# Kernel optimization log

Measured on AMD Instinct MI355X. Metric: run time of the kernel, lower is better.

The kernel has to match this reference:

```python
import jax, jax.numpy as jnp
import numpy as np

EM_DIM = 64
GROUP = 16
DIM_IN = 1024


def _position_embedding(boxes, part_boxes):
    # boxes: [N,4], part_boxes: [P,4] -> [N,P,EM_DIM]
    xmin, ymin, xmax, ymax = [boxes[:, i:i + 1] for i in range(4)]            # [N,1]
    pxmin, pymin, pxmax, pymax = [part_boxes[:, i:i + 1].T for i in range(4)]  # [1,P]
    bw = xmax - xmin + 1.0
    bh = ymax - ymin + 1.0
    pw = pxmax - pxmin + 1.0
    ph = pymax - pymin + 1.0
    cx = 0.5 * (xmin + xmax)
    cy = 0.5 * (ymin + ymax)
    pcx = 0.5 * (pxmin + pxmax)
    pcy = 0.5 * (pymin + pymax)
    dx = jnp.abs((cx - pcx) / bw)
    dy = jnp.abs((cy - pcy) / bh)
    dx = jnp.log(jnp.where(dx < 1e-3, 1e-3, dx))
    dy = jnp.log(jnp.where(dy < 1e-3, 1e-3, dy))
    dw = jnp.log(pw / bw)
    dh = jnp.log(ph / bh)
    pos = jnp.stack([dx, dy, dw, dh], axis=2)                                  # [N,P,4]
    em_range = jnp.arange(EM_DIM // 8, dtype=pos.dtype) / (EM_DIM // 8)        # [8]
    em_mat = jnp.power(jnp.asarray(1000.0, pos.dtype), em_range)               # [8]
    div = (100.0 * pos)[..., None] / em_mat                                    # [N,P,4,8]
    emb = jnp.concatenate([jnp.sin(div), jnp.cos(div)], axis=3)                # [N,P,4,16]
    return emb.reshape(pos.shape[0], pos.shape[1], EM_DIM)


def _single_relation(boxes, part_boxes, bf, pf, Wg_w, Wg_b, Wq_w, Wq_b, Wk_w, Wk_b, conv_w, conv_b):
    N = bf.shape[0]
    P = pf.shape[0]
    emb = _position_embedding(boxes, part_boxes)                               # [N,P,64]
    pos_feat = jax.nn.relu(emb @ Wg_w.T + Wg_b)                                # [N,P,G]
    att_weight = jnp.transpose(pos_feat, (0, 2, 1))                            # [N,G,P]
    q = (bf @ Wq_w.T + Wq_b).reshape(N, GROUP, EM_DIM)                         # [N,G,64]
    k = (pf @ Wk_w.T + Wk_b).reshape(P, GROUP, EM_DIM)                         # [P,G,64]
    att = jnp.einsum('ngd,pgd->ngp', q, k) * (1.0 / GROUP)                     # [N,G,P]
    att_weight = jnp.where(att_weight < 1e-6, 1e-6, att_weight)
    sm = jax.nn.softmax(jnp.log(att_weight) + att, axis=2)                     # [N,G,P]
    out = jnp.einsum('ngp,pc->ngc', sm, pf)                                    # [N,G,dim_in]
    # grouped 1x1 conv: group g maps dim_in channels -> EM_DIM channels
    w3 = conv_w.reshape(GROUP, EM_DIM, DIM_IN)
    rel = jnp.einsum('ngc,goc->ngo', out, w3).reshape(N, GROUP * EM_DIM) + conv_b
    return rel                                                                  # [N, G*EM_DIM]


def setup_inputs() -> dict:
    key = jax.random.key(0)
    ks = jax.random.split(key, 12)
    N_TOT, P_TOT = 2048, 2048

    def make_rois(k1, k2, n, n1):
        xy = jax.random.uniform(k1, (n, 2), jnp.float32) * 800.0
        wh = jax.random.uniform(k2, (n, 2), jnp.float32) * 200.0 + 16.0
        boxes = jnp.concatenate([xy, xy + wh], axis=1)
        idx = jnp.concatenate([jnp.zeros((n1, 1)), jnp.ones((n - n1, 1))], axis=0).astype(jnp.float32)
        return jnp.concatenate([idx, boxes], axis=1)

    rois = make_rois(ks[0], ks[1], N_TOT, 1024)
    part_rois = make_rois(ks[2], ks[3], P_TOT, 1024)
    box_feats = jax.random.normal(ks[4], (N_TOT, DIM_IN), jnp.float32)
    part_feats = jax.random.normal(ks[5], (P_TOT, DIM_IN), jnp.float32)
    xav_g = float(np.sqrt(6.0 / (EM_DIM + GROUP)))
    xav_qk = float(np.sqrt(6.0 / (DIM_IN + GROUP * EM_DIM)))
    Wg_w = jax.random.uniform(ks[6], (GROUP, EM_DIM), jnp.float32, -xav_g, xav_g)
    Wg_b = jnp.zeros((GROUP,), jnp.float32)
    Wq_w = jax.random.uniform(ks[7], (GROUP * EM_DIM, DIM_IN), jnp.float32, -xav_qk, xav_qk)
    Wq_b = jnp.zeros((GROUP * EM_DIM,), jnp.float32)
    Wk_w = jax.random.uniform(ks[8], (GROUP * EM_DIM, DIM_IN), jnp.float32, -xav_qk, xav_qk)
    Wk_b = jnp.zeros((GROUP * EM_DIM,), jnp.float32)
    conv_w = jax.random.normal(ks[9], (GROUP * EM_DIM, DIM_IN), jnp.float32) * 0.02
    conv_b = jnp.zeros((GROUP * EM_DIM,), jnp.float32)
    return {"rois": rois, "part_rois": part_rois, "box_feats": box_feats,
            "part_feats": part_feats, "Wg_w": Wg_w, "Wg_b": Wg_b,
            "Wq_w": Wq_w, "Wq_b": Wq_b, "Wk_w": Wk_w, "Wk_b": Wk_b,
            "conv_w": conv_w, "conv_b": conv_b, "n1_boxes": 1024, "n1_parts": 1024}


def reference(rois, part_rois, box_feats, part_feats, Wg_w, Wg_b, Wq_w, Wq_b,
              Wk_w, Wk_b, conv_w, conv_b, n1_boxes, n1_parts):
    boxes = rois[:, 1:5]
    part_boxes = part_rois[:, 1:5]
    params = (Wg_w, Wg_b, Wq_w, Wq_b, Wk_w, Wk_b, conv_w, conv_b)
    rel1 = _single_relation(boxes[:n1_boxes], part_boxes[:n1_parts],
                            box_feats[:n1_boxes], part_feats[:n1_parts], *params)
    rel2 = _single_relation(boxes[n1_boxes:], part_boxes[n1_parts:],
                            box_feats[n1_boxes:], part_feats[n1_parts:], *params)
    return jnp.concatenate([rel1, rel2], axis=0)  # [N_total, GROUP*EM_DIM]
```

## Files before the change

### kernel.cpp

```cpp
#include <hip/hip_runtime.h>

typedef unsigned short u16;
using short8  = __attribute__((ext_vector_type(8))) short;
using float4v = __attribute__((ext_vector_type(4))) float;

__device__ __forceinline__ u16 f2bf(float f) {
    union { float f; unsigned u; } v; v.f = f;
    unsigned r = (v.u + 0x7fff + ((v.u >> 16) & 1)) >> 16;
    return (u16)r;
}
__device__ __forceinline__ float bf2f(u16 h) {
    union { unsigned u; float f; } v; v.u = ((unsigned)h) << 16; return v.f;
}
__device__ __forceinline__ unsigned pkbf(float lo, float hi) {
    unsigned d;
    asm("v_cvt_pk_bf16_f32 %0, %1, %2" : "=v"(d) : "v"(lo), "v"(hi));
    return d;
}
__device__ __forceinline__ float sin_rev(float r) {
    float f, s;
    asm("v_fract_f32 %0, %1" : "=v"(f) : "v"(r));
    asm("v_sin_f32 %0, %1" : "=v"(s) : "v"(f));
    return s;
}
__device__ __forceinline__ void dma16(const void* g, void* l) {
    __builtin_amdgcn_global_load_lds((const __attribute__((address_space(1))) void*)g,
                                     (__attribute__((address_space(3))) void*)l, 16, 0, 0);
}

__device__ __forceinline__ void cvt4(const float* __restrict__ s, u16* __restrict__ o, int i) {
    float4 v = ((const float4*)s)[i];
    uint2 r; r.x = pkbf(v.x, v.y); r.y = pkbf(v.z, v.w);
    ((uint2*)o)[i] = r;
}

__global__ __launch_bounds__(256)
void cvt_all(const float* __restrict__ s0, const float* __restrict__ s1,
             const float* __restrict__ s2, const float* __restrict__ s3,
             const float* __restrict__ s4, const float* __restrict__ prois,
             u16* __restrict__ o0, u16* __restrict__ o1, u16* __restrict__ o2,
             u16* __restrict__ o3, u16* __restrict__ o4, float4* __restrict__ PD,
             int na4, int nb4, int nw4, int PT) {
    int i = blockIdx.x * 256 + threadIdx.x;
    if (i < na4) { cvt4(s0, o0, i); return; }
    i -= na4;
    if (i < nb4) { cvt4(s1, o1, i); return; }
    i -= nb4;
    if (i < nw4) { cvt4(s2, o2, i); return; }
    i -= nw4;
    if (i < nw4) { cvt4(s3, o3, i); return; }
    i -= nw4;
    if (i < nw4) { cvt4(s4, o4, i); return; }
    i -= nw4;
    if (i < PT) {
        const float* pr = prois + (size_t)i * 5;
        float pxmin = pr[1], pymin = pr[2], pxmax = pr[3], pymax = pr[4];
        PD[i] = make_float4(0.5f * (pxmin + pxmax), 0.5f * (pymin + pymax),
                            __logf(pxmax - pxmin + 1.0f), __logf(pymax - pymin + 1.0f));
    }
}

__global__ __launch_bounds__(256)
void proj_mfma(const u16* __restrict__ Ab, const u16* __restrict__ Pb,
               const u16* __restrict__ Wqb, const u16* __restrict__ Wkb,
               const u16* __restrict__ Cwb, const float* __restrict__ bq,
               const float* __restrict__ bk, u16* __restrict__ Qb,
               u16* __restrict__ Kb, u16* __restrict__ PVt, int PT) {
    __shared__ __align__(16) u16 As[128 * 64];
    __shared__ __align__(16) u16 Ws[64 * 64];
    __shared__ __align__(16) u16 Tr[128 * 68];

    const int z = blockIdx.z;
    const int m0 = blockIdx.y * 128, j0 = blockIdx.x * 64;
    const u16* A = (z == 0) ? Ab : Pb;
    const u16* W = (z == 0) ? Wqb : (z == 1 ? Wkb : Cwb);
    const int t = threadIdx.x;
    const int w = t >> 6, lane = t & 63;
    const int wm = w >> 1, wn = w & 1;
    const int lr = lane >> 3, lc = lane & 7, gch = lc ^ lr;
    const int fm = lane & 15, quad = lane >> 4;

    float4v zero4 = {0.f, 0.f, 0.f, 0.f};
    float4v acc[4][2];
#pragma unroll
    for (int i = 0; i < 4; ++i) { acc[i][0] = zero4; acc[i][1] = zero4; }

    for (int k0 = 0; k0 < 1024; k0 += 64) {
#pragma unroll
        for (int i = 0; i < 4; ++i) {
            int row = w * 32 + i * 8 + lr;
            dma16(A + (size_t)(m0 + row) * 1024 + k0 + gch * 8,
                  As + (w * 32 + i * 8) * 64 + lane * 8);
        }
#pragma unroll
        for (int i = 0; i < 2; ++i) {
            int row = w * 16 + i * 8 + lr;
            dma16(W + (size_t)(j0 + row) * 1024 + k0 + gch * 8,
                  Ws + (w * 16 + i * 8) * 64 + lane * 8);
        }
        __syncthreads();
#pragma unroll
        for (int ks = 0; ks < 2; ++ks) {
            int c = ks * 4 + quad;
            short8 af[4], bf[2];
#pragma unroll
            for (int i = 0; i < 4; ++i) {
                int ra = wm * 64 + i * 16 + fm;
                af[i] = *(const short8*)(As + ra * 64 + ((c ^ (ra & 7)) * 8));
            }
#pragma unroll
            for (int j = 0; j < 2; ++j) {
                int rb = wn * 32 + j * 16 + fm;
                bf[j] = *(const short8*)(Ws + rb * 64 + ((c ^ (rb & 7)) * 8));
            }
#pragma unroll
            for (int i = 0; i < 4; ++i)
#pragma unroll
                for (int j = 0; j < 2; ++j)
                    acc[i][j] = __builtin_amdgcn_mfma_f32_16x16x32_bf16(af[i], bf[j], acc[i][j], 0, 0, 0);
        }
        __syncthreads();
    }

    if (z < 2) {
        u16* O = z ? Kb : Qb;
        const float* bias = z ? bk : bq;
#pragma unroll
        for (int j = 0; j < 2; ++j) {
            int jl = wn * 32 + j * 16 + fm;
            float bb = bias[j0 + jl];
#pragma unroll
            for (int i = 0; i < 4; ++i) {
                int mlb = wm * 64 + i * 16 + quad * 4;
#pragma unroll
                for (int r = 0; r < 4; ++r)
                    Tr[(mlb + r) * 68 + jl] = f2bf(acc[i][j][r] + bb);
            }
        }
        __syncthreads();
#pragma unroll
        for (int i2 = 0; i2 < 4; ++i2) {
            int f = i2 * 2048 + t * 8;
            int ml = f >> 6, jl = f & 63;
            union { uint2 u2[2]; short8 s8; } uu;
            uu.u2[0] = *(const uint2*)(Tr + ml * 68 + jl);
            uu.u2[1] = *(const uint2*)(Tr + ml * 68 + jl + 4);
            *(short8*)(O + (size_t)(m0 + ml) * 1024 + j0 + jl) = uu.s8;
        }
    } else {
#pragma unroll
        for (int j = 0; j < 2; ++j) {
            int jl = wn * 32 + j * 16 + fm;
#pragma unroll
            for (int i = 0; i < 4; ++i) {
                int mlb = wm * 64 + i * 16 + quad * 4;
                uint2 pk;
                pk.x = pkbf(acc[i][j][0], acc[i][j][1]);
                pk.y = pkbf(acc[i][j][2], acc[i][j][3]);
                *(uint2*)(Tr + jl * 136 + mlb) = pk;
            }
        }
        __syncthreads();
#pragma unroll
        for (int i2 = 0; i2 < 4; ++i2) {
            int f = i2 * 2048 + t * 8;
            int jl = f >> 7, ml = f & 127;
            union { uint2 u2[2]; short8 s8; } uu;
            uu.u2[0] = *(const uint2*)(Tr + jl * 136 + ml);
            uu.u2[1] = *(const uint2*)(Tr + jl * 136 + ml + 4);
            *(short8*)(PVt + (size_t)(j0 + jl) * PT + m0 + ml) = uu.s8;
        }
    }
}

__global__ __launch_bounds__(256)
void att_mfma(const u16* __restrict__ Qb, const u16* __restrict__ Kb,
              u16* __restrict__ ATT, const int* __restrict__ n1b_p,
              const int* __restrict__ n1p_p, int PT) {
    __shared__ __align__(16) u16 Qs[128 * 64];
    __shared__ __align__(16) u16 Ks[128 * 64];
    __shared__ __align__(16) u16 Tr[128 * 130];

    const int g = blockIdx.z;
    const int n0 = blockIdx.y * 128, pl0 = blockIdx.x * 128;
    const int n1b = *n1b_p, n1p = *n1p_p;
    const int hh = (n0 >= n1b) ? 1 : 0;
    const int p0 = hh ? n1p : 0;
    const int Ph = hh ? (PT - n1p) : n1p;
    if (pl0 >= Ph) return;
    const int t = threadIdx.x;
    const int w = t >> 6, lane = t & 63;
    const int wm = w >> 1, wn = w & 1;
    const int lr = lane >> 3, lc = lane & 7, gch = lc ^ lr;
    const int fm = lane & 15, quad = lane >> 4;

    float4v zero4 = {0.f, 0.f, 0.f, 0.f};
    float4v acc[4][4];
#pragma unroll
    for (int i = 0; i < 4; ++i)
#pragma unroll
        for (int j = 0; j < 4; ++j) acc[i][j] = zero4;

#pragma unroll
    for (int i = 0; i < 4; ++i) {
        int row = w * 32 + i * 8 + lr;
        dma16(Qb + (size_t)(n0 + row) * 1024 + g * 64 + gch * 8,
              Qs + (w * 32 + i * 8) * 64 + lane * 8);
        dma16(Kb + (size_t)(p0 + pl0 + row) * 1024 + g * 64 + gch * 8,
              Ks + (w * 32 + i * 8) * 64 + lane * 8);
    }
    __syncthreads();
#pragma unroll
    for (int ks = 0; ks < 2; ++ks) {
        int c = ks * 4 + quad;
        short8 af[4], bf[4];
#pragma unroll
        for (int i = 0; i < 4; ++i) {
            int ra = wm * 64 + i * 16 + fm;
            af[i] = *(const short8*)(Qs + ra * 64 + ((c ^ (ra & 7)) * 8));
            int rb = wn * 64 + i * 16 + fm;
            bf[i] = *(const short8*)(Ks + rb * 64 + ((c ^ (rb & 7)) * 8));
        }
#pragma unroll
        for (int i = 0; i < 4; ++i)
#pragma unroll
            for (int j = 0; j < 4; ++j)
                acc[i][j] = __builtin_amdgcn_mfma_f32_16x16x32_bf16(af[i], bf[j], acc[i][j], 0, 0, 0);
    }
#pragma unroll
    for (int j = 0; j < 4; ++j) {
        int pl = wn * 64 + j * 16 + fm;
#pragma unroll
        for (int i = 0; i < 4; ++i)
#pragma unroll
            for (int r = 0; r < 4; ++r) {
                int nl = wm * 64 + i * 16 + quad * 4 + r;
                Tr[nl * 130 + pl] = f2bf(__expf(acc[i][j][r] * 0.0625f));
            }
    }
    __syncthreads();
#pragma unroll
    for (int i = 0; i < 8; ++i) {
        int f = i * 2048 + t * 8;
        int nl = f >> 7, pl = f & 127;
        short8 v = *(const short8*)(Tr + nl * 130 + pl);
        *(short8*)(ATT + ((size_t)(n0 + nl) * 16 + g) * 1024 + pl0 + pl) = v;
    }
}

__global__ __launch_bounds__(256)
void softmax_fused(const float* __restrict__ rois, const float4* __restrict__ PD,
                   const float* __restrict__ Wg_w, const float* __restrict__ Wg_b,
                   u16* __restrict__ ATT, float* __restrict__ INV,
                   const int* __restrict__ n1b_p, const int* __restrict__ n1p_p, int PT) {
    __shared__ float redl[4][16];

    const int n = blockIdx.x, t = threadIdx.x;
    const int w = t >> 6, lane = t & 63;
    const int fm = lane & 15, quad = lane >> 4;
    const int n1b = *n1b_p, n1p = *n1p_p;
    const int hh = (n >= n1b) ? 1 : 0;
    const int p0 = hh ? n1p : 0;
    const int Ph = hh ? (PT - n1p) : n1p;

    float xmin = rois[n * 5 + 1], ymin = rois[n * 5 + 2];
    float xmax = rois[n * 5 + 3], ymax = rois[n * 5 + 4];
    float bw = xmax - xmin + 1.0f, bh = ymax - ymin + 1.0f;
    float cx = 0.5f * (xmin + xmax), cy = 0.5f * (ymin + ymax);

    const int jA = quad >> 1, trig = quad & 1;
    float cA   = (jA == 0) ? cx : cy;
    float invA = (jA == 0) ? (1.0f / bw) : (1.0f / bh);
    float lB   = (jA == 0) ? __logf(bw) : __logf(bh);
    float toff = trig ? 0.25f : 0.0f;

    const int g_ = fm;
    short8 b1, b2;
    {
        const float* w1 = Wg_w + g_ * 64 + quad * 8;
        const float* w2 = Wg_w + g_ * 64 + 32 + quad * 8;
        unsigned* p1 = (unsigned*)&b1;
        unsigned* p2 = (unsigned*)&b2;
#pragma unroll
        for (int kk = 0; kk < 4; ++kk) {
            p1[kk] = pkbf(w1[2 * kk], w1[2 * kk + 1]);
            p2[kk] = pkbf(w2[2 * kk], w2[2 * kk + 1]);
        }
    }
    float wgb = Wg_b[g_];

    const float inv_em[8] = {1.0f, 0.4216965034f, 0.1778279410f, 0.0749894209f,
                             0.0316227766f, 0.0133352143f, 0.0056234133f, 0.0023713737f};
    const float REV = 15.91549431f;
    const int prange = Ph >> 2;
    const int pb0 = w * prange;
    float ssum = 0.0f;
    u16* rowp = ATT + ((size_t)n * 16 + g_) * 1024;

    float4 pd_c = PD[p0 + pb0 + fm];
    ushort4 ea_c = *(const ushort4*)(rowp + pb0 + quad * 4);

#pragma unroll 2
    for (int pt = 0; pt < 16; ++pt) {
        int pbase = pb0 + pt * 16;
        float4 pd_n;
        ushort4 ea_n;
        if (pt < 15) {
            pd_n = PD[p0 + pbase + 16 + fm];
            ea_n = *(const ushort4*)(rowp + pbase + 16 + quad * 4);
        }
        float pc = (jA == 0) ? pd_c.x : pd_c.y;
        float lp = (jA == 0) ? pd_c.z : pd_c.w;
        float posA = __logf(fmaxf(fabsf(cA - pc) * invA, 0.001f));
        float posB = lp - lB;
        float br1 = posA * REV, br2 = posB * REV;
        float e1[8], e2[8];
#pragma unroll
        for (int k = 0; k < 8; ++k) {
            e1[k] = sin_rev(fmaf(br1, inv_em[k], toff));
            e2[k] = sin_rev(fmaf(br2, inv_em[k], toff));
        }
        short8 a1, a2;
        unsigned* pa1 = (unsigned*)&a1;
        unsigned* pa2 = (unsigned*)&a2;
#pragma unroll
        for (int kk = 0; kk < 4; ++kk) {
            pa1[kk] = pkbf(e1[2 * kk], e1[2 * kk + 1]);
            pa2[kk] = pkbf(e2[2 * kk], e2[2 * kk + 1]);
        }
        float4v acc = {wgb, wgb, wgb, wgb};
        acc = __builtin_amdgcn_mfma_f32_16x16x32_bf16(a1, b1, acc, 0, 0, 0);
        acc = __builtin_amdgcn_mfma_f32_16x16x32_bf16(a2, b2, acc, 0, 0, 0);

        float w0  = fmaxf(acc[0], 1e-6f) * bf2f(ea_c.x);
        float w1v = fmaxf(acc[1], 1e-6f) * bf2f(ea_c.y);
        float w2v = fmaxf(acc[2], 1e-6f) * bf2f(ea_c.z);
        float w3v = fmaxf(acc[3], 1e-6f) * bf2f(ea_c.w);
        ssum += (w0 + w1v) + (w2v + w3v);
        uint2 wp; wp.x = pkbf(w0, w1v); wp.y = pkbf(w2v, w3v);
        *(uint2*)(rowp + pbase + quad * 4) = wp;

        pd_c = pd_n;
        ea_c = ea_n;
    }

    ssum += __shfl_xor(ssum, 16, 64);
    ssum += __shfl_xor(ssum, 32, 64);
    if (lane < 16) redl[w][lane] = ssum;
    __syncthreads();
    if (t < 16)
        INV[(size_t)n * 16 + t] = 1.0f / (redl[0][t] + redl[1][t] + redl[2][t] + redl[3][t]);
}

__global__ __launch_bounds__(256)
void rel_mfma(const u16* __restrict__ SM, const u16* __restrict__ PVt,
              const float* __restrict__ conv_b, const float* __restrict__ INV,
              float* __restrict__ OUT, const int* __restrict__ n1b_p,
              const int* __restrict__ n1p_p, int PT) {
    __shared__ __align__(16) u16 As[64 * 64];
    __shared__ __align__(16) u16 Bs[64 * 64];

    const int n0 = blockIdx.x * 64, g = blockIdx.y;
    const int n1b = *n1b_p, n1p = *n1p_p;
    const int hh = (n0 >= n1b) ? 1 : 0;
    const int p0 = hh ? n1p : 0;
    const int Ph = hh ? (PT - n1p) : n1p;
    const int t = threadIdx.x;
    const int w = t >> 6, lane = t & 63;
    const int wm = w >> 1, wn = w & 1;
    const int lr = lane >> 3, lc = lane & 7, gch = lc ^ lr;
    const int fm = lane & 15, quad = lane >> 4;

    float4v zero4 = {0.f, 0.f, 0.f, 0.f};
    float4v acc[2][2];
#pragma unroll
    for (int i = 0; i < 2; ++i) { acc[i][0] = zero4; acc[i][1] = zero4; }

    for (int k0 = 0; k0 < Ph; k0 += 64) {
#pragma unroll
        for (int i = 0; i < 2; ++i) {
            int row = w * 16 + i * 8 + lr;
            dma16(SM + ((size_t)(n0 + row) * 16 + g) * 1024 + k0 + gch * 8,
                  As + (w * 16 + i * 8) * 64 + lane * 8);
            dma16(PVt + (size_t)(g * 64 + row) * PT + p0 + k0 + gch * 8,
                  Bs + (w * 16 + i * 8) * 64 + lane * 8);
        }
        __syncthreads();
#pragma unroll
        for (int ks = 0; ks < 2; ++ks) {
            int c = ks * 4 + quad;
            short8 af[2], bf[2];
#pragma unroll
            for (int i = 0; i < 2; ++i) {
                int ra = wm * 32 + i * 16 + fm;
                af[i] = *(const short8*)(As + ra * 64 + ((c ^ (ra & 7)) * 8));
                int rb = wn * 32 + i * 16 + fm;
                bf[i] = *(const short8*)(Bs + rb * 64 + ((c ^ (rb & 7)) * 8));
            }
#pragma unroll
            for (int i = 0; i < 2; ++i)
#pragma unroll
                for (int j = 0; j < 2; ++j)
                    acc[i][j] = __builtin_amdgcn_mfma_f32_16x16x32_bf16(af[i], bf[j], acc[i][j], 0, 0, 0);
        }
        __syncthreads();
    }
    float bb[2];
    bb[0] = conv_b[g * 64 + wn * 32 + fm];
    bb[1] = conv_b[g * 64 + wn * 32 + 16 + fm];
#pragma unroll
    for (int i = 0; i < 2; ++i)
#pragma unroll
        for (int r = 0; r < 4; ++r) {
            int nn = n0 + wm * 32 + i * 16 + quad * 4 + r;
            float iv = INV[(size_t)nn * 16 + g];
#pragma unroll
            for (int j = 0; j < 2; ++j) {
                int o = wn * 32 + j * 16 + fm;
                OUT[(size_t)nn * 1024 + g * 64 + o] = acc[i][j][r] * iv + bb[j];
            }
        }
}

extern "C" void kernel_launch(void* const* d_in, const int* in_sizes, int n_in,
                              void* d_out, int out_size, void* d_ws, size_t ws_size,
                              hipStream_t stream) {
    const float* rois   = (const float*)d_in[0];
    const float* prois  = (const float*)d_in[1];
    const float* bfeat  = (const float*)d_in[2];
    const float* pfeat  = (const float*)d_in[3];
    const float* Wg_w   = (const float*)d_in[4];
    const float* Wg_b   = (const float*)d_in[5];
    const float* Wq_w   = (const float*)d_in[6];
    const float* Wq_b   = (const float*)d_in[7];
    const float* Wk_w   = (const float*)d_in[8];
    const float* Wk_b   = (const float*)d_in[9];
    const float* conv_w = (const float*)d_in[10];
    const float* conv_b = (const float*)d_in[11];
    const int*   n1b    = (const int*)d_in[12];
    const int*   n1p    = (const int*)d_in[13];

    const int NT = in_sizes[2] / 1024;
    const int PT = in_sizes[3] / 1024;

    u16* ATT = (u16*)d_ws;
    u16* Qb  = ATT + (size_t)NT * 16 * 1024;
    u16* Kb  = Qb + (size_t)NT * 1024;
    u16* PVt = Kb + (size_t)PT * 1024;
    float* INVp = (float*)(PVt + (size_t)1024 * PT);
    float4* PD  = (float4*)(INVp + (size_t)NT * 16);
    u16* Ab  = ATT;
    u16* Pb  = Ab + (size_t)NT * 1024;
    u16* Wqb = Pb + (size_t)PT * 1024;
    u16* Wkb = Wqb + 1024 * 1024;
    u16* Cwb = Wkb + 1024 * 1024;

    dim3 blk(256);
    int nf4 = NT * 1024 / 4, pf4 = PT * 1024 / 4, wf4 = 1024 * 1024 / 4;
    int tot = nf4 + pf4 + 3 * wf4 + PT;
    cvt_all<<<dim3((tot + 255) / 256), blk, 0, stream>>>(
        bfeat, pfeat, Wq_w, Wk_w, conv_w, prois, Ab, Pb, Wqb, Wkb, Cwb, PD,
        nf4, pf4, wf4, PT);

    proj_mfma<<<dim3(16, NT / 128, 3), blk, 0, stream>>>(Ab, Pb, Wqb, Wkb, Cwb,
                                                         Wq_b, Wk_b, Qb, Kb, PVt, PT);
    att_mfma<<<dim3(PT / 128, NT / 128, 16), blk, 0, stream>>>(Qb, Kb, ATT, n1b, n1p, PT);
    softmax_fused<<<dim3(NT), blk, 0, stream>>>(rois, PD, Wg_w, Wg_b, ATT, INVp, n1b, n1p, PT);
    rel_mfma<<<dim3(NT / 64, 16), blk, 0, stream>>>(ATT, PVt, conv_b, INVp,
                                                    (float*)d_out, n1b, n1p, PT);
}
```

Measured before the change: 202.8 us.

## Stage softmax attention row in LDS via async DMA and double block size

The softmax_fused kernel now copies each box's full 16x1024 bf16 attention block into shared memory with dma16 async copies at kernel start. It then does the read-modify-write of the positional weights against LDS and writes the whole block back to global memory with coalesced 16-byte stores. The block grows to 512 threads (8 waves), so each wave covers half as many parts. This aims to replace strided global loads and stores with bulk coalesced transfers and to add parallelism, at the cost of about 33 KB of LDS per block, which limits occupancy. A guard on prange skips tiles when Ph/8 is smaller than the loop bound.

```diff
diff --git a/kernel.cpp b/kernel.cpp
--- a/kernel.cpp
+++ b/kernel.cpp
@@ -248,12 +248,13 @@
     }
 }
 
-__global__ __launch_bounds__(256)
+__global__ __launch_bounds__(512)
 void softmax_fused(const float* __restrict__ rois, const float4* __restrict__ PD,
                    const float* __restrict__ Wg_w, const float* __restrict__ Wg_b,
                    u16* __restrict__ ATT, float* __restrict__ INV,
                    const int* __restrict__ n1b_p, const int* __restrict__ n1p_p, int PT) {
-    __shared__ float redl[4][16];
+    __shared__ __align__(16) u16 att_s[16 * 1032];
+    __shared__ float redl[8][16];
 
     const int n = blockIdx.x, t = threadIdx.x;
     const int w = t >> 6, lane = t & 63;
@@ -263,6 +264,16 @@
     const int p0 = hh ? n1p : 0;
     const int Ph = hh ? (PT - n1p) : n1p;
 
+    const u16* arow = ATT + (size_t)n * 16 * 1024;
+#pragma unroll
+    for (int i = 0; i < 4; ++i) {
+        int f = (i * 512 + t) * 16;
+        int g = f >> 11;
+        int off = f & 2047;
+        dma16((const char*)arow + g * 2048 + off,
+              (char*)att_s + g * 2064 + off);
+    }
+
     float xmin = rois[n * 5 + 1], ymin = rois[n * 5 + 2];
     float xmax = rois[n * 5 + 3], ymax = rois[n * 5 + 4];
     float bw = xmax - xmin + 1.0f, bh = ymax - ymin + 1.0f;
@@ -288,68 +299,78 @@
         }
     }
     float wgb = Wg_b[g_];
+    __syncthreads();
 
     const float inv_em[8] = {1.0f, 0.4216965034f, 0.1778279410f, 0.0749894209f,
                              0.0316227766f, 0.0133352143f, 0.0056234133f, 0.0023713737f};
     const float REV = 15.91549431f;
-    const int prange = Ph >> 2;
+    const int prange = Ph >> 3;
     const int pb0 = w * prange;
     float ssum = 0.0f;
-    u16* rowp = ATT + ((size_t)n * 16 + g_) * 1024;
+    u16* lrow = att_s + g_ * 1032;
 
     float4 pd_c = PD[p0 + pb0 + fm];
-    ushort4 ea_c = *(const ushort4*)(rowp + pb0 + quad * 4);
 
 #pragma unroll 2
-    for (int pt = 0; pt < 16; ++pt) {
+    for (int pt = 0; pt < 8; ++pt) {
         int pbase = pb0 + pt * 16;
-        float4 pd_n;
-        ushort4 ea_n;
-        if (pt < 15) {
-            pd_n = PD[p0 + pbase + 16 + fm];
-            ea_n = *(const ushort4*)(rowp + pbase + 16 + quad * 4);
-        }
-        float pc = (jA == 0) ? pd_c.x : pd_c.y;
-        float lp = (jA == 0) ? pd_c.z : pd_c.w;
-        float posA = __logf(fmaxf(fabsf(cA - pc) * invA, 0.001f));
-        float posB = lp - lB;
-        float br1 = posA * REV, br2 = posB * REV;
-        float e1[8], e2[8];
-#pragma unroll
-        for (int k = 0; k < 8; ++k) {
-            e1[k] = sin_rev(fmaf(br1, inv_em[k], toff));
-            e2[k] = sin_rev(fmaf(br2, inv_em[k], toff));
-        }
-        short8 a1, a2;
-        unsigned* pa1 = (unsigned*)&a1;
-        unsigned* pa2 = (unsigned*)&a2;
-#pragma unroll
-        for (int kk = 0; kk < 4; ++kk) {
-            pa1[kk] = pkbf(e1[2 * kk], e1[2 * kk + 1]);
-            pa2[kk] = pkbf(e2[2 * kk], e2[2 * kk + 1]);
-        }
-        float4v acc = {wgb, wgb, wgb, wgb};
-        acc = __builtin_amdgcn_mfma_f32_16x16x32_bf16(a1, b1, acc, 0, 0, 0);
-        acc = __builtin_amdgcn_mfma_f32_16x16x32_bf16(a2, b2, acc, 0, 0, 0);
-
-        float w0  = fmaxf(acc[0], 1e-6f) * bf2f(ea_c.x);
-        float w1v = fmaxf(acc[1], 1e-6f) * bf2f(ea_c.y);
-        float w2v = fmaxf(acc[2], 1e-6f) * bf2f(ea_c.z);
-        float w3v = fmaxf(acc[3], 1e-6f) * bf2f(ea_c.w);
-        ssum += (w0 + w1v) + (w2v + w3v);
-        uint2 wp; wp.x = pkbf(w0, w1v); wp.y = pkbf(w2v, w3v);
-        *(uint2*)(rowp + pbase + quad * 4) = wp;
-
-        pd_c = pd_n;
-        ea_c = ea_n;
+        if ((pt * 16) < prange) {
+            float4 pd_n;
+            if (pt < 7) pd_n = PD[p0 + pbase + 16 + fm];
+            float pc = (jA == 0) ? pd_c.x : pd_c.y;
+            float lp = (jA == 0) ? pd_c.z : pd_c.w;
+            float posA = __logf(fmaxf(fabsf(cA - pc) * invA, 0.001f));
+            float posB = lp - lB;
+            float br1 = posA * REV, br2 = posB * REV;
+            float e1[8], e2[8];
+#pragma unroll
+            for (int k = 0; k < 8; ++k) {
+                e1[k] = sin_rev(fmaf(br1, inv_em[k], toff));
+                e2[k] = sin_rev(fmaf(br2, inv_em[k], toff));
+            }
+            short8 a1, a2;
+            unsigned* pa1 = (unsigned*)&a1;
+            unsigned* pa2 = (unsigned*)&a2;
+#pragma unroll
+            for (int kk = 0; kk < 4; ++kk) {
+                pa1[kk] = pkbf(e1[2 * kk], e1[2 * kk + 1]);
+                pa2[kk] = pkbf(e2[2 * kk], e2[2 * kk + 1]);
+            }
+            float4v acc = {wgb, wgb, wgb, wgb};
+            acc = __builtin_amdgcn_mfma_f32_16x16x32_bf16(a1, b1, acc, 0, 0, 0);
+            acc = __builtin_amdgcn_mfma_f32_16x16x32_bf16(a2, b2, acc, 0, 0, 0);
+
+            u16* slot = lrow + pbase + quad * 4;
+            ushort4 ea = *(const ushort4*)slot;
+            float w0  = fmaxf(acc[0], 1e-6f) * bf2f(ea.x);
+            float w1v = fmaxf(acc[1], 1e-6f) * bf2f(ea.y);
+            float w2v = fmaxf(acc[2], 1e-6f) * bf2f(ea.z);
+            float w3v = fmaxf(acc[3], 1e-6f) * bf2f(ea.w);
+            ssum += (w0 + w1v) + (w2v + w3v);
+            uint2 wp; wp.x = pkbf(w0, w1v); wp.y = pkbf(w2v, w3v);
+            *(uint2*)slot = wp;
+            pd_c = pd_n;
+        }
     }
 
     ssum += __shfl_xor(ssum, 16, 64);
     ssum += __shfl_xor(ssum, 32, 64);
     if (lane < 16) redl[w][lane] = ssum;
     __syncthreads();
-    if (t < 16)
-        INV[(size_t)n * 16 + t] = 1.0f / (redl[0][t] + redl[1][t] + redl[2][t] + redl[3][t]);
+    if (t < 16) {
+        float s = 0.0f;
+#pragma unroll
+        for (int ww = 0; ww < 8; ++ww) s += redl[ww][t];
+        INV[(size_t)n * 16 + t] = 1.0f / s;
+    }
+
+#pragma unroll
+    for (int i = 0; i < 4; ++i) {
+        int f = (i * 512 + t) * 16;
+        int g = f >> 11, off = f & 2047;
+        short8 v = *(const short8*)((const char*)att_s + g * 2064 + off);
+        *(short8*)((char*)(ATT + (size_t)n * 16 * 1024) + g * 2048 + off) = v;
+    }
 }
 
 __global__ __launch_bounds__(256)
@@ -465,7 +486,7 @@
     proj_mfma<<<dim3(16, NT / 128, 3), blk, 0, stream>>>(Ab, Pb, Wqb, Wkb, Cwb,
                                                          Wq_b, Wk_b, Qb, Kb, PVt, PT);
     att_mfma<<<dim3(PT / 128, NT / 128, 16), blk, 0, stream>>>(Qb, Kb, ATT, n1b, n1p, PT);
-    softmax_fused<<<dim3(NT), blk, 0, stream>>>(rois, PD, Wg_w, Wg_b, ATT, INVp, n1b, n1p, PT);
+    softmax_fused<<<dim3(NT), dim3(512), 0, stream>>>(rois, PD, Wg_w, Wg_b, ATT, INVp, n1b, n1p, PT);
     rel_mfma<<<dim3(NT / 64, 16), blk, 0, stream>>>(ATT, PVt, conv_b, INVp,
                                                     (float*)d_out, n1b, n1p, PT);
 }
```

Measured after the change: 208.8 us. 3.0% more time.

## Split softmax kernel across four P-chunks with atomic row-sum accumulation

Applied to the files above, without the earlier changes.

The softmax/position-embedding kernel now launches four blocks per box row, each covering a quarter of the parts, instead of one block per row. Partial row sums are combined with atomicAdd into a buffer zeroed by the conversion kernel, and the consumer computes the reciprocal itself. The software prefetch of the attention values is dropped in favour of loading each slot right before it is updated. This raises the number of blocks and the parallelism in a memory-bound pass, at the cost of atomics and less latency hiding per wave.

```diff
diff --git a/kernel.cpp b/kernel.cpp
--- a/kernel.cpp
+++ b/kernel.cpp
@@ -40,7 +40,8 @@
              const float* __restrict__ s4, const float* __restrict__ prois,
              u16* __restrict__ o0, u16* __restrict__ o1, u16* __restrict__ o2,
              u16* __restrict__ o3, u16* __restrict__ o4, float4* __restrict__ PD,
-             int na4, int nb4, int nw4, int PT) {
+             float4* __restrict__ SUMz,
+             int na4, int nb4, int nw4, int PT, int ns4) {
     int i = blockIdx.x * 256 + threadIdx.x;
     if (i < na4) { cvt4(s0, o0, i); return; }
     i -= na4;
@@ -57,7 +58,10 @@
         float pxmin = pr[1], pymin = pr[2], pxmax = pr[3], pymax = pr[4];
         PD[i] = make_float4(0.5f * (pxmin + pxmax), 0.5f * (pymin + pymax),
                             __logf(pxmax - pxmin + 1.0f), __logf(pymax - pymin + 1.0f));
-    }
+        return;
+    }
+    i -= PT;
+    if (i < ns4) SUMz[i] = make_float4(0.f, 0.f, 0.f, 0.f);
 }
 
 __global__ __launch_bounds__(256)
@@ -249,10 +253,10 @@
 }
 
 __global__ __launch_bounds__(256)
-void softmax_fused(const float* __restrict__ rois, const float4* __restrict__ PD,
-                   const float* __restrict__ Wg_w, const float* __restrict__ Wg_b,
-                   u16* __restrict__ ATT, float* __restrict__ INV,
-                   const int* __restrict__ n1b_p, const int* __restrict__ n1p_p, int PT) {
+void softmax_part(const float* __restrict__ rois, const float4* __restrict__ PD,
+                  const float* __restrict__ Wg_w, const float* __restrict__ Wg_b,
+                  u16* __restrict__ ATT, float* __restrict__ SUM,
+                  const int* __restrict__ n1b_p, const int* __restrict__ n1p_p, int PT) {
     __shared__ float redl[4][16];
 
     const int n = blockIdx.x, t = threadIdx.x;
@@ -292,23 +296,19 @@
     const float inv_em[8] = {1.0f, 0.4216965034f, 0.1778279410f, 0.0749894209f,
                              0.0316227766f, 0.0133352143f, 0.0056234133f, 0.0023713737f};
     const float REV = 15.91549431f;
-    const int prange = Ph >> 2;
-    const int pb0 = w * prange;
+    const int chunk  = Ph >> 2;
+    const int wrange = chunk >> 2;
+    const int pb0 = blockIdx.y * chunk + w * wrange;
     float ssum = 0.0f;
     u16* rowp = ATT + ((size_t)n * 16 + g_) * 1024;
 
     float4 pd_c = PD[p0 + pb0 + fm];
-    ushort4 ea_c = *(const ushort4*)(rowp + pb0 + quad * 4);
 
 #pragma unroll 2
-    for (int pt = 0; pt < 16; ++pt) {
+    for (int pt = 0; pt * 16 < wrange; ++pt) {
         int pbase = pb0 + pt * 16;
         float4 pd_n;
-        ushort4 ea_n;
-        if (pt < 15) {
-            pd_n = PD[p0 + pbase + 16 + fm];
-            ea_n = *(const ushort4*)(rowp + pbase + 16 + quad * 4);
-        }
+        if ((pt + 1) * 16 < wrange) pd_n = PD[p0 + pbase + 16 + fm];
         float pc = (jA == 0) ? pd_c.x : pd_c.y;
         float lp = (jA == 0) ? pd_c.z : pd_c.w;
         float posA = __logf(fmaxf(fabsf(cA - pc) * invA, 0.001f));
@@ -332,29 +332,31 @@
         acc = __builtin_amdgcn_mfma_f32_16x16x32_bf16(a1, b1, acc, 0, 0, 0);
         acc = __builtin_amdgcn_mfma_f32_16x16x32_bf16(a2, b2, acc, 0, 0, 0);
 
-        float w0  = fmaxf(acc[0], 1e-6f) * bf2f(ea_c.x);
-        float w1v = fmaxf(acc[1], 1e-6f) * bf2f(ea_c.y);
-        float w2v = fmaxf(acc[2], 1e-6f) * bf2f(ea_c.z);
-        float w3v = fmaxf(acc[3], 1e-6f) * bf2f(ea_c.w);
+        u16* slot = rowp + pbase + quad * 4;
+        ushort4 ea = *(const ushort4*)slot;
+        float w0  = fmaxf(acc[0], 1e-6f) * bf2f(ea.x);
+        float w1v = fmaxf(acc[1], 1e-6f) * bf2f(ea.y);
+        float w2v = fmaxf(acc[2], 1e-6f) * bf2f(ea.z);
+        float w3v = fmaxf(acc[3], 1e-6f) * bf2f(ea.w);
         ssum += (w0 + w1v) + (w2v + w3v);
         uint2 wp; wp.x = pkbf(w0, w1v); wp.y = pkbf(w2v, w3v);
-        *(uint2*)(rowp + pbase + quad * 4) = wp;
-
+        *(uint2*)slot = wp;
         pd_c = pd_n;
-        ea_c = ea_n;
     }
 
     ssum += __shfl_xor(ssum, 16, 64);
     ssum += __shfl_xor(ssum, 32, 64);
     if (lane < 16) redl[w][lane] = ssum;
     __syncthreads();
-    if (t < 16)
-        INV[(size_t)n * 16 + t] = 1.0f / (redl[0][t] + redl[1][t] + redl[2][t] + redl[3][t]);
+    if (t < 16) {
+        float s = redl[0][t] + redl[1][t] + redl[2][t] + redl[3][t];
+        atomicAdd(&SUM[(size_t)n * 16 + t], s);
+    }
 }
 
 __global__ __launch_bounds__(256)
 void rel_mfma(const u16* __restrict__ SM, const u16* __restrict__ PVt,
-              const float* __restrict__ conv_b, const float* __restrict__ INV,
+              const float* __restrict__ conv_b, const float* __restrict__ SUM,
               float* __restrict__ OUT, const int* __restrict__ n1b_p,
               const int* __restrict__ n1p_p, int PT) {
     __shared__ __align__(16) u16 As[64 * 64];
@@ -413,7 +415,7 @@
 #pragma unroll
         for (int r = 0; r < 4; ++r) {
             int nn = n0 + wm * 32 + i * 16 + quad * 4 + r;
-            float iv = INV[(size_t)nn * 16 + g];
+            float iv = 1.0f / SUM[(size_t)nn * 16 + g];
 #pragma unroll
             for (int j = 0; j < 2; ++j) {
                 int o = wn * 32 + j * 16 + fm;
@@ -447,8 +449,8 @@
     u16* Qb  = ATT + (size_t)NT * 16 * 1024;
     u16* Kb  = Qb + (size_t)NT * 1024;
     u16* PVt = Kb + (size_t)PT * 1024;
-    float* INVp = (float*)(PVt + (size_t)1024 * PT);
-    float4* PD  = (float4*)(INVp + (size_t)NT * 16);
+    float* SUMp = (float*)(PVt + (size_t)1024 * PT);
+    float4* PD  = (float4*)(SUMp + (size_t)NT * 16);
     u16* Ab  = ATT;
     u16* Pb  = Ab + (size_t)NT * 1024;
     u16* Wqb = Pb + (size_t)PT * 1024;
@@ -457,15 +459,16 @@
 
     dim3 blk(256);
     int nf4 = NT * 1024 / 4, pf4 = PT * 1024 / 4, wf4 = 1024 * 1024 / 4;
-    int tot = nf4 + pf4 + 3 * wf4 + PT;
+    int ns4 = NT * 16 / 4;
+    int tot = nf4 + pf4 + 3 * wf4 + PT + ns4;
     cvt_all<<<dim3((tot + 255) / 256), blk, 0, stream>>>(
         bfeat, pfeat, Wq_w, Wk_w, conv_w, prois, Ab, Pb, Wqb, Wkb, Cwb, PD,
-        nf4, pf4, wf4, PT);
+        (float4*)SUMp, nf4, pf4, wf4, PT, ns4);
 
     proj_mfma<<<dim3(16, NT / 128, 3), blk, 0, stream>>>(Ab, Pb, Wqb, Wkb, Cwb,
                                                          Wq_b, Wk_b, Qb, Kb, PVt, PT);
     att_mfma<<<dim3(PT / 128, NT / 128, 16), blk, 0, stream>>>(Qb, Kb, ATT, n1b, n1p, PT);
-    softmax_fused<<<dim3(NT), blk, 0, stream>>>(rois, PD, Wg_w, Wg_b, ATT, INVp, n1b, n1p, PT);
-    rel_mfma<<<dim3(NT / 64, 16), blk, 0, stream>>>(ATT, PVt, conv_b, INVp,
+    softmax_part<<<dim3(NT, 4), blk, 0, stream>>>(rois, PD, Wg_w, Wg_b, ATT, SUMp, n1b, n1p, PT);
+    rel_mfma<<<dim3(NT / 64, 16), blk, 0, stream>>>(ATT, PVt, conv_b, SUMp,
                                                     (float*)d_out, n1b, n1p, PT);
 }
```

Result: slower. 211.6 us (+4.3%).

## Precompute part-size sinusoids and fold box-size phase into Wg weights via angle addition

Applied to the files above, without the earlier changes.

The dw/dh embedding terms depend on log(pw) - log(bw). Angle-addition identities split them into a per-part sin/cos table, built once in the conversion kernel and stored as bf16, and a per-box rotation folded into the second MFMA's B weights. The softmax kernel then loads 16 bytes of precomputed A-fragment per part instead of evaluating 8 sin ops per element, which halves its transcendental work. The cost is an extra global table read, and bf16 rounding now happens at a different point in the calculation, which may slightly change accuracy.

```diff
diff --git a/kernel.cpp b/kernel.cpp
--- a/kernel.cpp
+++ b/kernel.cpp
@@ -28,6 +28,10 @@
                                      (__attribute__((address_space(3))) void*)l, 16, 0, 0);
 }
 
+__constant__ float c_inv_em[8] = {1.0f, 0.4216965034f, 0.1778279410f, 0.0749894209f,
+                                  0.0316227766f, 0.0133352143f, 0.0056234133f, 0.0023713737f};
+#define REVC 15.91549431f
+
 __device__ __forceinline__ void cvt4(const float* __restrict__ s, u16* __restrict__ o, int i) {
     float4 v = ((const float4*)s)[i];
     uint2 r; r.x = pkbf(v.x, v.y); r.y = pkbf(v.z, v.w);
@@ -39,7 +43,8 @@
              const float* __restrict__ s2, const float* __restrict__ s3,
              const float* __restrict__ s4, const float* __restrict__ prois,
              u16* __restrict__ o0, u16* __restrict__ o1, u16* __restrict__ o2,
-             u16* __restrict__ o3, u16* __restrict__ o4, float4* __restrict__ PD,
+             u16* __restrict__ o3, u16* __restrict__ o4,
+             float2* __restrict__ PD1, u16* __restrict__ PD2,
              int na4, int nb4, int nw4, int PT) {
     int i = blockIdx.x * 256 + threadIdx.x;
     if (i < na4) { cvt4(s0, o0, i); return; }
@@ -55,8 +60,24 @@
     if (i < PT) {
         const float* pr = prois + (size_t)i * 5;
         float pxmin = pr[1], pymin = pr[2], pxmax = pr[3], pymax = pr[4];
-        PD[i] = make_float4(0.5f * (pxmin + pxmax), 0.5f * (pymin + pymax),
-                            __logf(pxmax - pxmin + 1.0f), __logf(pymax - pymin + 1.0f));
+        PD1[i] = make_float2(0.5f * (pxmin + pxmax), 0.5f * (pymin + pymax));
+        float lpw = __logf(pxmax - pxmin + 1.0f);
+        float lph = __logf(pymax - pymin + 1.0f);
+        u16 out[32];
+#pragma unroll
+        for (int k = 0; k < 8; ++k) {
+            float pw_ = REVC * c_inv_em[k] * lpw;
+            float ph_ = REVC * c_inv_em[k] * lph;
+            out[k]      = f2bf(sin_rev(pw_));
+            out[8 + k]  = f2bf(sin_rev(pw_ + 0.25f));
+            out[16 + k] = f2bf(sin_rev(ph_));
+            out[24 + k] = f2bf(sin_rev(ph_ + 0.25f));
+        }
+        u16* dst = PD2 + (size_t)i * 32;
+#pragma unroll
+        for (int q = 0; q < 4; ++q)
+            *(ushort4*)(dst + q * 8 + 0) = make_ushort4(out[q*8], out[q*8+1], out[q*8+2], out[q*8+3]),
+            *(ushort4*)(dst + q * 8 + 4) = make_ushort4(out[q*8+4], out[q*8+5], out[q*8+6], out[q*8+7]);
     }
 }
 
@@ -249,7 +270,8 @@
 }
 
 __global__ __launch_bounds__(256)
-void softmax_fused(const float* __restrict__ rois, const float4* __restrict__ PD,
+void softmax_fused(const float* __restrict__ rois, const float2* __restrict__ PD1,
+                   const u16* __restrict__ PD2,
                    const float* __restrict__ Wg_w, const float* __restrict__ Wg_b,
                    u16* __restrict__ ATT, float* __restrict__ INV,
                    const int* __restrict__ n1b_p, const int* __restrict__ n1p_p, int PT) {
@@ -268,69 +290,74 @@
     float bw = xmax - xmin + 1.0f, bh = ymax - ymin + 1.0f;
     float cx = 0.5f * (xmin + xmax), cy = 0.5f * (ymin + ymax);
 
-    const int jA = quad >> 1, trig = quad & 1;
-    float cA   = (jA == 0) ? cx : cy;
-    float invA = (jA == 0) ? (1.0f / bw) : (1.0f / bh);
-    float lB   = (jA == 0) ? __logf(bw) : __logf(bh);
-    float toff = trig ? 0.25f : 0.0f;
+    const int sel = quad >> 1, which = quad & 1;
+    float cA   = sel ? cy : cx;
+    float invA = sel ? (1.0f / bh) : (1.0f / bw);
+    float lB   = sel ? __logf(bh) : __logf(bw);
+    float toff = which ? 0.25f : 0.0f;
 
     const int g_ = fm;
-    short8 b1, b2;
+    short8 b1;
     {
         const float* w1 = Wg_w + g_ * 64 + quad * 8;
-        const float* w2 = Wg_w + g_ * 64 + 32 + quad * 8;
         unsigned* p1 = (unsigned*)&b1;
+#pragma unroll
+        for (int kk = 0; kk < 4; ++kk)
+            p1[kk] = pkbf(w1[2 * kk], w1[2 * kk + 1]);
+    }
+    short8 b2;
+    {
+        const float* ws_ = Wg_w + g_ * 64 + 32 + sel * 16;
+        const float* wc_ = ws_ + 8;
+        float vb[8];
+#pragma unroll
+        for (int k = 0; k < 8; ++k) {
+            float psi = REVC * c_inv_em[k] * lB;
+            float s = sin_rev(psi), c = sin_rev(psi + 0.25f);
+            float a = ws_[k], b = wc_[k];
+            vb[k] = which ? (b * c - a * s) : (a * c + b * s);
+        }
         unsigned* p2 = (unsigned*)&b2;
 #pragma unroll
-        for (int kk = 0; kk < 4; ++kk) {
-            p1[kk] = pkbf(w1[2 * kk], w1[2 * kk + 1]);
-            p2[kk] = pkbf(w2[2 * kk], w2[2 * kk + 1]);
-        }
+        for (int kk = 0; kk < 4; ++kk)
+            p2[kk] = pkbf(vb[2 * kk], vb[2 * kk + 1]);
     }
     float wgb = Wg_b[g_];
 
-    const float inv_em[8] = {1.0f, 0.4216965034f, 0.1778279410f, 0.0749894209f,
-                             0.0316227766f, 0.0133352143f, 0.0056234133f, 0.0023713737f};
-    const float REV = 15.91549431f;
+    const float REV = REVC;
     const int prange = Ph >> 2;
     const int pb0 = w * prange;
     float ssum = 0.0f;
     u16* rowp = ATT + ((size_t)n * 16 + g_) * 1024;
 
-    float4 pd_c = PD[p0 + pb0 + fm];
+    float   pc_c = ((const float*)PD1)[(size_t)(p0 + pb0 + fm) * 2 + sel];
+    short8  a2_c = *(const short8*)(PD2 + (size_t)(p0 + pb0 + fm) * 32 + quad * 8);
     ushort4 ea_c = *(const ushort4*)(rowp + pb0 + quad * 4);
 
 #pragma unroll 2
     for (int pt = 0; pt < 16; ++pt) {
         int pbase = pb0 + pt * 16;
-        float4 pd_n;
-        ushort4 ea_n;
+        float pc_n; short8 a2_n; ushort4 ea_n;
         if (pt < 15) {
-            pd_n = PD[p0 + pbase + 16 + fm];
+            pc_n = ((const float*)PD1)[(size_t)(p0 + pbase + 16 + fm) * 2 + sel];
+            a2_n = *(const short8*)(PD2 + (size_t)(p0 + pbase + 16 + fm) * 32 + quad * 8);
             ea_n = *(const ushort4*)(rowp + pbase + 16 + quad * 4);
         }
-        float pc = (jA == 0) ? pd_c.x : pd_c.y;
-        float lp = (jA == 0) ? pd_c.z : pd_c.w;
-        float posA = __logf(fmaxf(fabsf(cA - pc) * invA, 0.001f));
-        float posB = lp - lB;
-        float br1 = posA * REV, br2 = posB * REV;
-        float e1[8], e2[8];
-#pragma unroll
-        for (int k = 0; k < 8; ++k) {
-            e1[k] = sin_rev(fmaf(br1, inv_em[k], toff));
-            e2[k] = sin_rev(fmaf(br2, inv_em[k], toff));
-        }
-        short8 a1, a2;
+        float posA = __logf(fmaxf(fabsf(cA - pc_c) * invA, 0.001f));
+        float br1 = posA * REV;
+        float e1[8];
+#pragma unroll
+        for (int k = 0; k < 8; ++k)
+            e1[k] = sin_rev(fmaf(br1, c_inv_em[k], toff));
+        short8 a1;
         unsigned* pa1 = (unsigned*)&a1;
-        unsigned* pa2 = (unsigned*)&a2;
-#pragma unroll
-        for (int kk = 0; kk < 4; ++kk) {
+#pragma unroll
+        for (int kk = 0; kk < 4; ++kk)
             pa1[kk] = pkbf(e1[2 * kk], e1[2 * kk + 1]);
-            pa2[kk] = pkbf(e2[2 * kk], e2[2 * kk + 1]);
-        }
+
         float4v acc = {wgb, wgb, wgb, wgb};
         acc = __builtin_amdgcn_mfma_f32_16x16x32_bf16(a1, b1, acc, 0, 0, 0);
-        acc = __builtin_amdgcn_mfma_f32_16x16x32_bf16(a2, b2, acc, 0, 0, 0);
+        acc = __builtin_amdgcn_mfma_f32_16x16x32_bf16(a2_c, b2, acc, 0, 0, 0);
 
         float w0  = fmaxf(acc[0], 1e-6f) * bf2f(ea_c.x);
         float w1v = fmaxf(acc[1], 1e-6f) * bf2f(ea_c.y);
@@ -340,8 +367,7 @@
         uint2 wp; wp.x = pkbf(w0, w1v); wp.y = pkbf(w2v, w3v);
         *(uint2*)(rowp + pbase + quad * 4) = wp;
 
-        pd_c = pd_n;
-        ea_c = ea_n;
+        pc_c = pc_n; a2_c = a2_n; ea_c = ea_n;
     }
 
     ssum += __shfl_xor(ssum, 16, 64);
@@ -448,7 +474,8 @@
     u16* Kb  = Qb + (size_t)NT * 1024;
     u16* PVt = Kb + (size_t)PT * 1024;
     float* INVp = (float*)(PVt + (size_t)1024 * PT);
-    float4* PD  = (float4*)(INVp + (size_t)NT * 16);
+    float2* PD1 = (float2*)(INVp + (size_t)NT * 16);
+    u16* PD2 = (u16*)(PD1 + PT);
     u16* Ab  = ATT;
     u16* Pb  = Ab + (size_t)NT * 1024;
     u16* Wqb = Pb + (size_t)PT * 1024;
@@ -459,13 +486,13 @@
     int nf4 = NT * 1024 / 4, pf4 = PT * 1024 / 4, wf4 = 1024 * 1024 / 4;
     int tot = nf4 + pf4 + 3 * wf4 + PT;
     cvt_all<<<dim3((tot + 255) / 256), blk, 0, stream>>>(
-        bfeat, pfeat, Wq_w, Wk_w, conv_w, prois, Ab, Pb, Wqb, Wkb, Cwb, PD,
-        nf4, pf4, wf4, PT);
+        bfeat, pfeat, Wq_w, Wk_w, conv_w, prois, Ab, Pb, Wqb, Wkb, Cwb,
+        PD1, PD2, nf4, pf4, wf4, PT);
 
     proj_mfma<<<dim3(16, NT / 128, 3), blk, 0, stream>>>(Ab, Pb, Wqb, Wkb, Cwb,
                                                          Wq_b, Wk_b, Qb, Kb, PVt, PT);
     att_mfma<<<dim3(PT / 128, NT / 128, 16), blk, 0, stream>>>(Qb, Kb, ATT, n1b, n1p, PT);
-    softmax_fused<<<dim3(NT), blk, 0, stream>>>(rois, PD, Wg_w, Wg_b, ATT, INVp, n1b, n1p, PT);
+    softmax_fused<<<dim3(NT), blk, 0, stream>>>(rois, PD1, PD2, Wg_w, Wg_b, ATT, INVp, n1b, n1p, PT);
     rel_mfma<<<dim3(NT / 64, 16), blk, 0, stream>>>(ATT, PVt, conv_b, INVp,
                                                     (float*)d_out, n1b, n1p, PT);
 }
```

Result: slower. 209.3 us (+3.2%).
